# Optimization experiments

Measured on AMD Instinct MI355X. Metric: run time of the kernel, lower is better.

Reference implementation:

```python
import jax, jax.numpy as jnp
import numpy as np

EMB = 1024
HEADS = 16
DK = EMB // HEADS

def setup_inputs() -> dict:
    key = jax.random.key(0)
    ks = jax.random.split(key, 5)
    scale = 0.02
    return {
        "x": jax.random.normal(ks[0], (4, 2048, EMB), dtype=jnp.float32),
        "W_in": jax.random.normal(ks[1], (3 * EMB, EMB), dtype=jnp.float32) * scale,
        "b_in": jax.random.normal(ks[2], (3 * EMB,), dtype=jnp.float32) * scale,
        "W_out": jax.random.normal(ks[3], (EMB, EMB), dtype=jnp.float32) * scale,
        "b_out": jax.random.normal(ks[4], (EMB,), dtype=jnp.float32) * scale,
    }

def reference(x, W_in, b_in, W_out, b_out):
    B, T, C = x.shape
    qkv = x @ W_in.T + b_in                      # [B,T,3C]
    q, k, v = jnp.split(qkv, 3, axis=-1)
    def heads(t):
        return t.reshape(B, T, HEADS, DK).transpose(0, 2, 1, 3)  # [B,H,T,Dk]
    q, k, v = heads(q), heads(k), heads(v)
    scores = jnp.einsum("bhqd,bhkd->bhqk", q, k) / jnp.sqrt(jnp.float32(DK))
    causal = jnp.tril(jnp.ones((T, T), dtype=bool))
    scores = jnp.where(causal, scores, jnp.finfo(scores.dtype).min)
    attn = jax.nn.softmax(scores, axis=-1)
    y = jnp.einsum("bhqk,bhkd->bhqd", attn, v)   # [B,H,T,Dk]
    y = y.transpose(0, 2, 1, 3).reshape(B, T, C)
    return y @ W_out.T + b_out
```

## Files before the change

### kernel.cpp

```cpp
#include <hip/hip_runtime.h>
#include <hip/hip_bf16.h>

#define EMB   1024
#define HEADS 16
#define DKV   64
#define BB    4
#define TT    2048
#define MTOT  8192

#define QSCALE 0.1803368801111204f
#define RESCALE_THR 8.0f

typedef short bf16x8 __attribute__((ext_vector_type(8)));
typedef float f32x4  __attribute__((ext_vector_type(4)));

__device__ __forceinline__ ushort bf16_bits(float f) {
    union { __hip_bfloat16 h; ushort u; } cv;
    cv.h = __float2bfloat16(f);
    return cv.u;
}
__device__ __forceinline__ unsigned pack_bf16(float lo, float hi) {
    return (unsigned)bf16_bits(lo) | ((unsigned)bf16_bits(hi) << 16);
}
__device__ __forceinline__ void gload16(const void* g, void* lds) {
    __builtin_amdgcn_global_load_lds(
        (const __attribute__((address_space(1))) unsigned*)g,
        (__attribute__((address_space(3))) unsigned*)lds, 16, 0, 0);
}
__device__ __forceinline__ int swz128(int row, int bytecol) {
    return row * 128 + (bytecol ^ ((row & 7) << 4));
}

__global__ void cvt_all(const float* __restrict__ x,   ushort* __restrict__ xo,
                        const float* __restrict__ wi,  ushort* __restrict__ wio,
                        const float* __restrict__ wo,  ushort* __restrict__ woo) {
    const int n4x = (MTOT * EMB) / 4;
    const int n4i = (3 * EMB * EMB) / 4;
    const int n4o = (EMB * EMB) / 4;
    int idx = blockIdx.x * blockDim.x + threadIdx.x;
    int stride = gridDim.x * blockDim.x;
    for (int i = idx; i < n4x + n4i + n4o; i += stride) {
        const float* in;
        ushort* out;
        int j = i;
        if (j < n4x)            { in = x;  out = xo;  }
        else if (j < n4x + n4i) { in = wi; out = wio; j -= n4x; }
        else                    { in = wo; out = woo; j -= n4x + n4i; }
        float4 v = reinterpret_cast<const float4*>(in)[j];
        ushort4 o;
        o.x = bf16_bits(v.x);
        o.y = bf16_bits(v.y);
        o.z = bf16_bits(v.z);
        o.w = bf16_bits(v.w);
        reinterpret_cast<ushort4*>(out)[j] = o;
    }
}

template<int EPI>
__global__ __launch_bounds__(256) void gemm_bt(
    const ushort* __restrict__ Ab, const ushort* __restrict__ Wb,
    const float* __restrict__ bias,
    ushort* __restrict__ qo, ushort* __restrict__ ko, ushort* __restrict__ vo,
    float* __restrict__ outf,
    int Msz, int Nsz, int Ksz)
{
    __shared__ __align__(16) ushort Sh[4][128 * 32];

    int tid = threadIdx.x;
    int mtiles = Msz >> 7;
    int bm = blockIdx.x % mtiles;
    int bn = blockIdx.x / mtiles;
    int m0 = bm << 7, n0 = bn << 7;
    int w = tid >> 6, l = tid & 63;
    int wr = w >> 1, wc = w & 1;
    int lr = l & 15, lk = (l >> 4) << 3;
    int srow = w * 16 + (l >> 2);
    int scol = (l & 3) << 3;

    f32x4 acc[4][4] = {};

    auto STAGE = [&](int buf, int k0) {
        #pragma unroll
        for (int p = 0; p < 2; ++p) {
            int row = p * 64 + srow;
            gload16(&Ab[(size_t)(m0 + row) * Ksz + k0 + scol],
                    (char*)Sh[buf * 2]     + (size_t)(p * 256 + w * 64) * 16);
            gload16(&Wb[(size_t)(n0 + row) * Ksz + k0 + scol],
                    (char*)Sh[buf * 2 + 1] + (size_t)(p * 256 + w * 64) * 16);
        }
    };

    STAGE(0, 0);
    int buf = 0;
    for (int k0 = 0; k0 < Ksz; k0 += 32) {
        __syncthreads();
        if (k0 + 32 < Ksz) STAGE(buf ^ 1, k0 + 32);
        const ushort* As = Sh[buf * 2];
        const ushort* Bs = Sh[buf * 2 + 1];

        bf16x8 a[4], b[4];
        #pragma unroll
        for (int mi = 0; mi < 4; ++mi)
            a[mi] = *(const bf16x8*)(&As[(wr * 64 + mi * 16 + lr) * 32 + lk]);
        #pragma unroll
        for (int ni = 0; ni < 4; ++ni)
            b[ni] = *(const bf16x8*)(&Bs[(wc * 64 + ni * 16 + lr) * 32 + lk]);
        __builtin_amdgcn_s_setprio(1);
        #pragma unroll
        for (int mi = 0; mi < 4; ++mi)
            #pragma unroll
            for (int ni = 0; ni < 4; ++ni)
                acc[mi][ni] = __builtin_amdgcn_mfma_f32_16x16x32_bf16(
                    a[mi], b[ni], acc[mi][ni], 0, 0, 0);
        __builtin_amdgcn_s_setprio(0);
        buf ^= 1;
    }

    if (EPI == 1) {
        #pragma unroll
        for (int mi = 0; mi < 4; ++mi)
            #pragma unroll
            for (int ni = 0; ni < 4; ++ni) {
                int n = n0 + wc * 64 + ni * 16 + lr;
                float bv = bias[n];
                #pragma unroll
                for (int r = 0; r < 4; ++r) {
                    int m = m0 + wr * 64 + mi * 16 + ((l >> 4) << 2) + r;
                    outf[(size_t)m * Nsz + n] = acc[mi][ni][r] + bv;
                }
            }
    } else {
        int which = n0 >> 10;
        if (which < 2) {
            ushort* dst = (which == 0) ? qo : ko;
            float qs = (which == 0) ? QSCALE : 1.f;
            #pragma unroll
            for (int mi = 0; mi < 4; ++mi)
                #pragma unroll
                for (int ni = 0; ni < 4; ++ni) {
                    int n = n0 + wc * 64 + ni * 16 + lr;
                    float bv = bias[n];
                    int rem = n & 1023;
                    int hd = rem >> 6, dk = rem & 63;
                    #pragma unroll
                    for (int r = 0; r < 4; ++r) {
                        int m = m0 + wr * 64 + mi * 16 + ((l >> 4) << 2) + r;
                        int b_ = m >> 11, t_ = m & 2047;
                        dst[((((size_t)b_ * HEADS + hd) * TT + t_) << 6) + dk] =
                            bf16_bits((acc[mi][ni][r] + bv) * qs);
                    }
                }
        } else {
            char* Tb = (char*)Sh;
            int b_ = m0 >> 11;
            int row_r = tid >> 1;
            int rem = (n0 + row_r) & 1023;
            int hd = rem >> 6, dk = rem & 63;
            size_t vrow = ((size_t)(b_ * HEADS + hd) * DKV + dk) * TT;
            int tbase = (m0 & 2047) + (tid & 1) * 32;
            #pragma unroll
            for (int h = 0; h < 2; ++h) {
                __syncthreads();
                if (wr == h) {
                    #pragma unroll
                    for (int ni = 0; ni < 4; ++ni) {
                        int n_l = wc * 64 + ni * 16 + lr;
                        float bv = bias[n0 + n_l];
                        #pragma unroll
                        for (int mi = 0; mi < 4; ++mi) {
                            uint2 u;
                            u.x = pack_bf16(acc[mi][ni][0] + bv, acc[mi][ni][1] + bv);
                            u.y = pack_bf16(acc[mi][ni][2] + bv, acc[mi][ni][3] + bv);
                            *(uint2*)(Tb + swz128(n_l, mi * 32 + ((l >> 4) << 3))) = u;
                        }
                    }
                }
                __syncthreads();
                #pragma unroll
                for (int qq = 0; qq < 4; ++qq) {
                    int4 d = *(const int4*)(Tb + swz128(row_r, (tid & 1) * 64 + qq * 16));
                    *(int4*)(&vo[vrow + tbase + h * 64 + qq * 8]) = d;
                }
            }
        }
    }
}

__device__ __forceinline__ void strip_tile(
    const char* __restrict__ Kbuf, const char* __restrict__ Vbuf, char* __restrict__ Plw,
    bf16x8 q0, bf16x8 q1,
    float& m_run, float& l_run, f32x4 (&o)[4],
    int lr, int g, bool diag, int qloc)
{
    f32x4 st[4];
    #pragma unroll
    for (int kt = 0; kt < 4; ++kt) {
        bf16x8 a0 = *(const bf16x8*)(Kbuf + swz128(kt * 16 + lr, g * 16));
        bf16x8 a1 = *(const bf16x8*)(Kbuf + swz128(kt * 16 + lr, 64 + g * 16));
        f32x4 z = {};
        z = __builtin_amdgcn_mfma_f32_16x16x32_bf16(a0, q0, z, 0, 0, 0);
        z = __builtin_amdgcn_mfma_f32_16x16x32_bf16(a1, q1, z, 0, 0, 0);
        st[kt] = z;
    }
    if (diag) {
        #pragma unroll
        for (int kt = 0; kt < 4; ++kt)
            #pragma unroll
            for (int r = 0; r < 4; ++r) {
                int kvloc = kt * 16 + g * 4 + r;
                st[kt][r] = (kvloc <= qloc) ? st[kt][r] : -1e30f;
            }
    }
    float mx = -1e30f;
    #pragma unroll
    for (int kt = 0; kt < 4; ++kt)
        #pragma unroll
        for (int r = 0; r < 4; ++r) mx = fmaxf(mx, st[kt][r]);
    mx = fmaxf(mx, __shfl_xor(mx, 16));
    mx = fmaxf(mx, __shfl_xor(mx, 32));

    if (!__all(mx - m_run <= RESCALE_THR)) {
        float mnew = fmaxf(m_run, mx);
        float alpha = exp2f(m_run - mnew);
        m_run = mnew;
        l_run *= alpha;
        float al0 = __shfl(alpha, g * 4 + 0);
        float al1 = __shfl(alpha, g * 4 + 1);
        float al2 = __shfl(alpha, g * 4 + 2);
        float al3 = __shfl(alpha, g * 4 + 3);
        #pragma unroll
        for (int dt = 0; dt < 4; ++dt) {
            o[dt][0] *= al0; o[dt][1] *= al1; o[dt][2] *= al2; o[dt][3] *= al3;
        }
    }

    float rs = 0.f;
    #pragma unroll
    for (int kt = 0; kt < 4; ++kt) {
        float p0 = exp2f(st[kt][0] - m_run);
        float p1 = exp2f(st[kt][1] - m_run);
        float p2 = exp2f(st[kt][2] - m_run);
        float p3 = exp2f(st[kt][3] - m_run);
        rs += (p0 + p1) + (p2 + p3);
        uint2 u;
        u.x = pack_bf16(p0, p1);
        u.y = pack_bf16(p2, p3);
        *(uint2*)(Plw + swz128(lr, kt * 32 + g * 8)) = u;
    }
    rs += __shfl_xor(rs, 16);
    rs += __shfl_xor(rs, 32);
    l_run += rs;

    bf16x8 pa0 = *(const bf16x8*)(Plw + swz128(lr, g * 16));
    bf16x8 pa1 = *(const bf16x8*)(Plw + swz128(lr, 64 + g * 16));

    #pragma unroll
    for (int dt = 0; dt < 4; ++dt) {
        bf16x8 b0 = *(const bf16x8*)(Vbuf + swz128(dt * 16 + lr, g * 16));
        bf16x8 b1 = *(const bf16x8*)(Vbuf + swz128(dt * 16 + lr, 64 + g * 16));
        o[dt] = __builtin_amdgcn_mfma_f32_16x16x32_bf16(pa0, b0, o[dt], 0, 0, 0);
        o[dt] = __builtin_amdgcn_mfma_f32_16x16x32_bf16(pa1, b1, o[dt], 0, 0, 0);
    }
}

__global__ __launch_bounds__(256, 3) void attn_kernel(
    const ushort* __restrict__ qb, const ushort* __restrict__ kb,
    const ushort* __restrict__ vtb, ushort* __restrict__ yb)
{
    __shared__ __align__(16) char Ks[2][64 * 128];
    __shared__ __align__(16) char Vs[2][64 * 128];
    __shared__ __align__(16) char Pl[4][16 * 128];

    int tid = threadIdx.x;
    int w = tid >> 6, l = tid & 63;
    int bid = blockIdx.x;
    int swz = (bid & 7) * 128 + (bid >> 3);
    int pair = swz & 15;
    int bh = swz >> 4;
    int qtA = 31 - pair, qtB = pair;

    const ushort* Q  = qb  + (size_t)bh * TT * DKV;
    const ushort* K  = kb  + (size_t)bh * TT * DKV;
    const ushort* Vt = vtb + (size_t)bh * DKV * TT;
    int lr = l & 15, g = l >> 4;
    int qA0 = qtA * 64 + w * 16;
    int qB0 = qtB * 64 + w * 16;

    bf16x8 qaA0 = *(const bf16x8*)(&Q[(size_t)(qA0 + lr) * DKV + g * 8]);
    bf16x8 qaA1 = *(const bf16x8*)(&Q[(size_t)(qA0 + lr) * DKV + 32 + g * 8]);
    bf16x8 qaB0 = *(const bf16x8*)(&Q[(size_t)(qB0 + lr) * DKV + g * 8]);
    bf16x8 qaB1 = *(const bf16x8*)(&Q[(size_t)(qB0 + lr) * DKV + 32 + g * 8]);

    int srow = w * 8 + (l >> 3);
    int scel = ((((l & 7) * 16) ^ ((l >> 3) << 4)) >> 1);

    float mA = -1e30f, lA = 0.f, mB = -1e30f, lB = 0.f;
    f32x4 oA[4] = {}, oB[4] = {};
    int nt = qtA + 1;

    #pragma unroll
    for (int p = 0; p < 2; ++p) {
        int row = p * 32 + srow;
        gload16(&K [(size_t)row * DKV + scel], (char*)Ks[0] + (size_t)(p * 256 + w * 64) * 16);
        gload16(&Vt[(size_t)row * TT  + scel], (char*)Vs[0] + (size_t)(p * 256 + w * 64) * 16);
    }

    for (int jt = 0; jt < nt; ++jt) {
        int buf = jt & 1;
        __syncthreads();

        if (jt + 1 < nt) {
            int kv1 = (jt + 1) * 64;
            #pragma unroll
            for (int p = 0; p < 2; ++p) {
                int row = p * 32 + srow;
                gload16(&K [(size_t)(kv1 + row) * DKV + scel],
                        (char*)Ks[buf ^ 1] + (size_t)(p * 256 + w * 64) * 16);
                gload16(&Vt[(size_t)row * TT + kv1 + scel],
                        (char*)Vs[buf ^ 1] + (size_t)(p * 256 + w * 64) * 16);
            }
        }

        strip_tile(Ks[buf], Vs[buf], Pl[w], qaA0, qaA1, mA, lA, oA,
                   lr, g, jt == qtA, w * 16 + lr);
        if (jt <= qtB)
            strip_tile(Ks[buf], Vs[buf], Pl[w], qaB0, qaB1, mB, lB, oB,
                       lr, g, jt == qtB, w * 16 + lr);
    }

    int b_ = bh >> 4, h_ = bh & 15;
    {
        float li0 = 1.f / __shfl(lA, g * 4 + 0);
        float li1 = 1.f / __shfl(lA, g * 4 + 1);
        float li2 = 1.f / __shfl(lA, g * 4 + 2);
        float li3 = 1.f / __shfl(lA, g * 4 + 3);
        #pragma unroll
        for (int dt = 0; dt < 4; ++dt) {
            int d_ = h_ * 64 + dt * 16 + lr;
            size_t base = ((size_t)b_ * TT + (qA0 + g * 4)) * EMB + d_;
            yb[base]           = bf16_bits(oA[dt][0] * li0);
            yb[base + EMB]     = bf16_bits(oA[dt][1] * li1);
            yb[base + 2 * EMB] = bf16_bits(oA[dt][2] * li2);
            yb[base + 3 * EMB] = bf16_bits(oA[dt][3] * li3);
        }
    }
    {
        float li0 = 1.f / __shfl(lB, g * 4 + 0);
        float li1 = 1.f / __shfl(lB, g * 4 + 1);
        float li2 = 1.f / __shfl(lB, g * 4 + 2);
        float li3 = 1.f / __shfl(lB, g * 4 + 3);
        #pragma unroll
        for (int dt = 0; dt < 4; ++dt) {
            int d_ = h_ * 64 + dt * 16 + lr;
            size_t base = ((size_t)b_ * TT + (qB0 + g * 4)) * EMB + d_;
            yb[base]           = bf16_bits(oB[dt][0] * li0);
            yb[base + EMB]     = bf16_bits(oB[dt][1] * li1);
            yb[base + 2 * EMB] = bf16_bits(oB[dt][2] * li2);
            yb[base + 3 * EMB] = bf16_bits(oB[dt][3] * li3);
        }
    }
}

extern "C" void kernel_launch(void* const* d_in, const int* in_sizes, int n_in,
                              void* d_out, int out_size, void* d_ws, size_t ws_size,
                              hipStream_t stream) {
    const float* x     = (const float*)d_in[0];
    const float* W_in  = (const float*)d_in[1];
    const float* b_in  = (const float*)d_in[2];
    const float* W_out = (const float*)d_in[3];
    const float* b_out = (const float*)d_in[4];
    float* out = (float*)d_out;
    char* ws = (char*)d_ws;

    ushort* xb  = (ushort*)(ws);
    ushort* wib = (ushort*)(ws + 16777216);
    ushort* wob = (ushort*)(ws + 23068672);
    ushort* qbp = (ushort*)(ws + 25165824);
    ushort* kbp = (ushort*)(ws + 41943040);
    ushort* vbp = (ushort*)(ws + 58720256);
    ushort* ybp = (ushort*)(ws + 75497472);

    cvt_all<<<1280, 256, 0, stream>>>(x, xb, W_in, wib, W_out, wob);

    gemm_bt<0><<<dim3((MTOT / 128) * (3 * EMB / 128)), dim3(256), 0, stream>>>(
        xb, wib, b_in, qbp, kbp, vbp, nullptr, MTOT, 3 * EMB, EMB);

    attn_kernel<<<dim3(BB * HEADS * 16), dim3(256), 0, stream>>>(
        qbp, kbp, vbp, ybp);

    gemm_bt<1><<<dim3((MTOT / 128) * (EMB / 128)), dim3(256), 0, stream>>>(
        ybp, wob, b_out, nullptr, nullptr, nullptr, out, MTOT, EMB, EMB);
}
```

Before: 192.9 us.

## Load V directly from global into registers, drop V LDS staging, raise occupancy

```diff
diff --git a/kernel.cpp b/kernel.cpp
--- a/kernel.cpp
+++ b/kernel.cpp
@@ -187,7 +187,8 @@
 }
 
 __device__ __forceinline__ void strip_tile(
-    const char* __restrict__ Kbuf, const char* __restrict__ Vbuf, char* __restrict__ Plw,
+    const char* __restrict__ Kbuf, const ushort* __restrict__ Vt, int kv0,
+    char* __restrict__ Plw,
     bf16x8 q0, bf16x8 q1,
     float& m_run, float& l_run, f32x4 (&o)[4],
     int lr, int g, bool diag, int qloc)
@@ -198,9 +199,18 @@
         bf16x8 a0 = *(const bf16x8*)(Kbuf + swz128(kt * 16 + lr, g * 16));
         bf16x8 a1 = *(const bf16x8*)(Kbuf + swz128(kt * 16 + lr, 64 + g * 16));
         f32x4 z = {};
+        __builtin_amdgcn_s_setprio(1);
         z = __builtin_amdgcn_mfma_f32_16x16x32_bf16(a0, q0, z, 0, 0, 0);
         z = __builtin_amdgcn_mfma_f32_16x16x32_bf16(a1, q1, z, 0, 0, 0);
+        __builtin_amdgcn_s_setprio(0);
         st[kt] = z;
+    }
+    bf16x8 vb0[4], vb1[4];
+    #pragma unroll
+    for (int dt = 0; dt < 4; ++dt) {
+        const ushort* Vrow = Vt + (size_t)(dt * 16 + lr) * TT + kv0 + g * 8;
+        vb0[dt] = *(const bf16x8*)(Vrow);
+        vb1[dt] = *(const bf16x8*)(Vrow + 32);
     }
     if (diag) {
         #pragma unroll
@@ -254,21 +264,20 @@
     bf16x8 pa0 = *(const bf16x8*)(Plw + swz128(lr, g * 16));
     bf16x8 pa1 = *(const bf16x8*)(Plw + swz128(lr, 64 + g * 16));
 
+    __builtin_amdgcn_s_setprio(1);
     #pragma unroll
     for (int dt = 0; dt < 4; ++dt) {
-        bf16x8 b0 = *(const bf16x8*)(Vbuf + swz128(dt * 16 + lr, g * 16));
-        bf16x8 b1 = *(const bf16x8*)(Vbuf + swz128(dt * 16 + lr, 64 + g * 16));
-        o[dt] = __builtin_amdgcn_mfma_f32_16x16x32_bf16(pa0, b0, o[dt], 0, 0, 0);
-        o[dt] = __builtin_amdgcn_mfma_f32_16x16x32_bf16(pa1, b1, o[dt], 0, 0, 0);
-    }
-}
-
-__global__ __launch_bounds__(256, 3) void attn_kernel(
+        o[dt] = __builtin_amdgcn_mfma_f32_16x16x32_bf16(pa0, vb0[dt], o[dt], 0, 0, 0);
+        o[dt] = __builtin_amdgcn_mfma_f32_16x16x32_bf16(pa1, vb1[dt], o[dt], 0, 0, 0);
+    }
+    __builtin_amdgcn_s_setprio(0);
+}
+
+__global__ __launch_bounds__(256, 4) void attn_kernel(
     const ushort* __restrict__ qb, const ushort* __restrict__ kb,
     const ushort* __restrict__ vtb, ushort* __restrict__ yb)
 {
     __shared__ __align__(16) char Ks[2][64 * 128];
-    __shared__ __align__(16) char Vs[2][64 * 128];
     __shared__ __align__(16) char Pl[4][16 * 128];
 
     int tid = threadIdx.x;
@@ -301,30 +310,28 @@
     #pragma unroll
     for (int p = 0; p < 2; ++p) {
         int row = p * 32 + srow;
-        gload16(&K [(size_t)row * DKV + scel], (char*)Ks[0] + (size_t)(p * 256 + w * 64) * 16);
-        gload16(&Vt[(size_t)row * TT  + scel], (char*)Vs[0] + (size_t)(p * 256 + w * 64) * 16);
+        gload16(&K[(size_t)row * DKV + scel], (char*)Ks[0] + (size_t)(p * 256 + w * 64) * 16);
     }
 
     for (int jt = 0; jt < nt; ++jt) {
         int buf = jt & 1;
+        int kv0 = jt * 64;
         __syncthreads();
 
         if (jt + 1 < nt) {
-            int kv1 = (jt + 1) * 64;
+            int kv1 = kv0 + 64;
             #pragma unroll
             for (int p = 0; p < 2; ++p) {
                 int row = p * 32 + srow;
-                gload16(&K [(size_t)(kv1 + row) * DKV + scel],
+                gload16(&K[(size_t)(kv1 + row) * DKV + scel],
                         (char*)Ks[buf ^ 1] + (size_t)(p * 256 + w * 64) * 16);
-                gload16(&Vt[(size_t)row * TT + kv1 + scel],
-                        (char*)Vs[buf ^ 1] + (size_t)(p * 256 + w * 64) * 16);
             }
         }
 
-        strip_tile(Ks[buf], Vs[buf], Pl[w], qaA0, qaA1, mA, lA, oA,
+        strip_tile(Ks[buf], Vt, kv0, Pl[w], qaA0, qaA1, mA, lA, oA,
                    lr, g, jt == qtA, w * 16 + lr);
         if (jt <= qtB)
-            strip_tile(Ks[buf], Vs[buf], Pl[w], qaB0, qaB1, mB, lB, oB,
+            strip_tile(Ks[buf], Vt, kv0, Pl[w], qaB0, qaB1, mB, lB, oB,
                        lr, g, jt == qtB, w * 16 + lr);
     }
 
```

After: 246.1 us. +27.6%, slower.
